# Kernel tuning notes

Measured on AMD Instinct MI355X. Metric: run time of the kernel, lower is better.

Reference implementation:

```python
import jax, jax.numpy as jnp
import numpy as np

DIM = 3
N_GRID = 128
DX = 1.0 / N_GRID
INV_DX = float(N_GRID)
DT = 1e-4
P_VOL = (DX * 0.5) ** 2
P_RHO = 1.0
P_MASS = P_VOL * P_RHO
E_MOD = 5000.0
NU = 0.2
MU0 = E_MOD / (2.0 * (1.0 + NU))
LAM0 = E_MOD * NU / ((1.0 + NU) * (1.0 - 2.0 * NU))
N_PARTICLES = 400_000

# 27 stencil offsets of the quadratic B-spline kernel
_OFF = jnp.array([[i, j, k] for i in range(3) for j in range(3) for k in range(3)],
                 dtype=jnp.int32)  # [27,3]


def _substep(x, v, C, F, Jp, gravity, attractor_strength, attractor_pos, material):
    N = x.shape[0]
    dtype = x.dtype
    I3 = jnp.eye(3, dtype=dtype)

    # ---- particle -> grid (P2G) ----
    base = jnp.floor(x * INV_DX - 0.5).astype(jnp.int32)          # [N,3]
    fx = x * INV_DX - base.astype(dtype)                          # [N,3]
    # quadratic kernel weights, w[a, n, d], a in {0,1,2}
    w = jnp.stack([0.5 * (1.5 - fx) ** 2,
                   0.75 - (fx - 1.0) ** 2,
                   0.5 * (fx - 0.5) ** 2], axis=0)                # [3,N,3]

    Fn = jnp.einsum('nij,njk->nik', I3 + DT * C, F)               # deformation update

    h = jnp.clip(jnp.exp(10.0 * (1.0 - Jp)), 0.1, 5.0)
    h = jnp.where(material == 1, 0.3, h)
    mu = jnp.where(material == 0, 0.0, MU0 * h)                   # [N]
    la = LAM0 * h                                                 # [N]

    U, s, Vh = jnp.linalg.svd(Fn, full_matrices=False)            # [N,3,3],[N,3],[N,3,3]

    # faithful to source: plasticity loop only touches first TWO singular values
    J = jnp.ones_like(Jp)
    sig = s
    for d in range(2):
        new_sig = jnp.where(material == 2,
                            jnp.clip(s[:, d], 1.0 - 0.025, 1.0 + 0.0045),
                            s[:, d])
        Jp = Jp * s[:, d] / new_sig
        sig = sig.at[:, d].set(new_sig)
        J = J * new_sig

    F_fluid = jnp.sqrt(J)[:, None, None] * I3                     # material 0
    F_snow = jnpum = None
    F_snow = jnp.einsum('nij,nj,njk->nik', U, sig, Vh)            # material 2: U diag(sig) V^T
    m3 = material[:, None, None]
    Fn = jnp.where(m3 == 0, F_fluid, jnp.where(m3 == 2, F_snow, Fn))

    R = jnp.einsum('nij,njk->nik', U, Vh)                         # U V^T (rotation)
    stress = (2.0 * mu[:, None, None] * jnp.einsum('nij,nkj->nik', Fn - R, Fn)
              + I3 * (la * J * (J - 1.0))[:, None, None])
    stress = (-DT * P_VOL * 4.0 * INV_DX * INV_DX) * stress
    affine = stress + P_MASS * C                                  # [N,3,3]

    # NOTE faithful quirk of the source: weight = w[i][0] * w[j][1] (k-component unused)
    weight = w[_OFF[:, 0], :, 0] * w[_OFF[:, 1], :, 1]            # [27,N]
    dpos = (_OFF[:, None, :].astype(dtype) - fx[None]) * DX       # [27,N,3]
    mom = weight[..., None] * (P_MASS * v[None]
                               + jnp.einsum('nij,onj->oni', affine, dpos))  # [27,N,3]

    idx = base[None] + _OFF[:, None, :]                           # [27,N,3]
    flat = (idx[..., 0] * N_GRID + idx[..., 1]) * N_GRID + idx[..., 2]      # [27,N]
    G3 = N_GRID ** 3
    grid_mom = jnp.zeros((G3, 3), dtype).at[flat.reshape(-1)].add(mom.reshape(-1, 3))
    grid_m = jnp.zeros((G3,), dtype).at[flat.reshape(-1)].add((weight * P_MASS).reshape(-1))

    # ---- grid update ----
    a = jnp.arange(N_GRID, dtype=jnp.int32)
    coords = jnp.stack(jnp.meshgrid(a, a, a, indexing='ij'), axis=-1).reshape(G3, 3)
    mask = grid_m > 0
    m_safe = jnp.where(mask, grid_m, 1.0)
    gv = grid_mom / m_safe[:, None]
    gv = gv + DT * gravity * 30.0
    dist = attractor_pos[None, :] - DX * coords.astype(dtype)
    gv = gv + dist / (0.01 + jnp.linalg.norm(dist, axis=-1, keepdims=True)) \
              * attractor_strength * DT * 100.0
    ic, jc = coords[:, 0], coords[:, 1]
    vx, vy, vz = gv[:, 0], gv[:, 1], gv[:, 2]
    vx = jnp.where((ic < 3) & (vx < 0), 0.0, vx)
    vx = jnp.where((ic > N_GRID - 3) & (vx > 0), 0.0, vx)
    vy = jnp.where((jc < 3) & (vy < 0), 0.0, vy)
    vy = jnp.where((jc > N_GRID - 3) & (vy > 0), 0.0, vy)
    gv = jnp.stack([vx, vy, vz], axis=-1)
    gv = jnp.where(mask[:, None], gv, 0.0)                        # untouched cells stay zero

    # ---- grid -> particle (G2P) ----
    g_v = gv[flat]                                                # [27,N,3]
    dpos2 = _OFF[:, None, :].astype(dtype) - fx[None]             # [27,N,3] (no dx scale)
    new_v = jnp.einsum('on,onc->nc', weight, g_v)                 # [N,3]
    new_C = 4.0 * INV_DX * jnp.einsum('on,onc,ond->ncd', weight, g_v, dpos2)  # [N,3,3]
    x_new = x + DT * new_v

    # pack state: [x(3) | v(3) | Jp(1) | F(9) | C(9)] -> [N,25]
    return jnp.concatenate([x_new, new_v, Jp[:, None],
                            Fn.reshape(N, 9), new_C.reshape(N, 9)], axis=1)


def setup_inputs() -> dict:
    key = jax.random.key(0)
    ks = jax.random.split(key, 9)
    N = N_PARTICLES
    x = 0.1 + 0.8 * jax.random.uniform(ks[0], (N, 3), dtype=jnp.float32)
    v = 0.1 * jax.random.normal(ks[1], (N, 3), dtype=jnp.float32)
    C = 0.01 * jax.random.normal(ks[2], (N, 3, 3), dtype=jnp.float32)
    F = jnp.eye(3, dtype=jnp.float32) + 0.01 * jax.random.normal(ks[3], (N, 3, 3), dtype=jnp.float32)
    Jp = 1.0 + 0.1 * jax.random.uniform(ks[4], (N,), dtype=jnp.float32)
    material = jax.random.randint(ks[5], (N,), 0, 3, dtype=jnp.int32)
    gravity = jnp.array([0.0, -1.0, 0.0], dtype=jnp.float32)
    attractor_strength = jax.random.uniform(ks[6], (), dtype=jnp.float32)
    attractor_pos = jax.random.uniform(ks[7], (3,), dtype=jnp.float32)
    return {"x": x, "v": v, "C": C, "F": F, "Jp": Jp,
            "gravity": gravity, "attractor_strength": attractor_strength,
            "attractor_pos": attractor_pos, "material": material}


def reference(x, v, C, F, Jp, gravity, attractor_strength, attractor_pos, material):
    return _substep(x, v, C, F, Jp, gravity, attractor_strength, attractor_pos, material)
```

## Files before the change

kernel.cpp:

```cpp
#include <hip/hip_runtime.h>

#define NG 128
#define G3 (NG*NG*NG)
#define NSCAN_BLOCKS (G3/256)

__device__ __constant__ const float c_DX      = 1.0f/128.0f;
__device__ __constant__ const float c_INV_DX  = 128.0f;

#define DT      1e-4f
#define P_VOL   ((1.0f/256.0f)*(1.0f/256.0f))
#define P_MASS  P_VOL
#define MU0     (5000.0f/(2.0f*1.2f))
#define LAM0    (5000.0f*0.2f/(1.2f*0.6f))

struct __align__(16) PRec {
    float4 r0, r1, r2, r3;
};

template<int P, int Q>
__device__ inline void jacobi_rot(float S[3][3], float V[3][3]) {
    float apq = S[P][Q];
    if (fabsf(apq) < 1e-24f) return;
    float tau = (S[Q][Q] - S[P][P]) / (2.0f * apq);
    float t = copysignf(1.0f, tau) / (fabsf(tau) + sqrtf(1.0f + tau*tau));
    float c = rsqrtf(1.0f + t*t);
    float sn = t * c;
    #pragma unroll
    for (int k = 0; k < 3; ++k) {
        float Spk = S[P][k], Sqk = S[Q][k];
        S[P][k] = c*Spk - sn*Sqk;
        S[Q][k] = sn*Spk + c*Sqk;
    }
    #pragma unroll
    for (int k = 0; k < 3; ++k) {
        float Skp = S[k][P], Skq = S[k][Q];
        S[k][P] = c*Skp - sn*Skq;
        S[k][Q] = sn*Skp + c*Skq;
    }
    #pragma unroll
    for (int k = 0; k < 3; ++k) {
        float Vkp = V[k][P], Vkq = V[k][Q];
        V[k][P] = c*Vkp - sn*Vkq;
        V[k][Q] = sn*Vkp + c*Vkq;
    }
}

#define CSWAPF(cond, x, y) { float _t = (x); (x) = (cond) ? (y) : (x); (y) = (cond) ? _t : (y); }

__device__ inline void svd3(const float A[9], float U[9], float sv[3], float V[9]) {
    float S[3][3];
    #pragma unroll
    for (int i = 0; i < 3; ++i)
        #pragma unroll
        for (int j = 0; j < 3; ++j) {
            float acc = 0.f;
            #pragma unroll
            for (int k = 0; k < 3; ++k) acc += A[k*3+i]*A[k*3+j];
            S[i][j] = acc;
        }
    float Vm[3][3] = {{1.f,0.f,0.f},{0.f,1.f,0.f},{0.f,0.f,1.f}};
    #pragma unroll
    for (int sweep = 0; sweep < 4; ++sweep) {
        jacobi_rot<0,1>(S, Vm);
        jacobi_rot<0,2>(S, Vm);
        jacobi_rot<1,2>(S, Vm);
    }
    float l0 = S[0][0], l1 = S[1][1], l2 = S[2][2];
    float a0 = Vm[0][0], b0 = Vm[1][0], c0 = Vm[2][0];
    float a1 = Vm[0][1], b1 = Vm[1][1], c1 = Vm[2][1];
    float a2 = Vm[0][2], b2 = Vm[1][2], c2 = Vm[2][2];
    bool s01 = l0 < l1;
    CSWAPF(s01, l0, l1) CSWAPF(s01, a0, a1) CSWAPF(s01, b0, b1) CSWAPF(s01, c0, c1)
    bool s02 = l0 < l2;
    CSWAPF(s02, l0, l2) CSWAPF(s02, a0, a2) CSWAPF(s02, b0, b2) CSWAPF(s02, c0, c2)
    bool s12 = l1 < l2;
    CSWAPF(s12, l1, l2) CSWAPF(s12, a1, a2) CSWAPF(s12, b1, b2) CSWAPF(s12, c1, c2)

    {
        float l = fmaxf(l0, 0.f); float sval = sqrtf(l); sv[0] = sval;
        V[0] = a0; V[3] = b0; V[6] = c0;
        float inv = (sval > 1e-12f) ? 1.0f/sval : 0.f;
        U[0] = (A[0]*a0 + A[1]*b0 + A[2]*c0)*inv;
        U[3] = (A[3]*a0 + A[4]*b0 + A[5]*c0)*inv;
        U[6] = (A[6]*a0 + A[7]*b0 + A[8]*c0)*inv;
    }
    {
        float l = fmaxf(l1, 0.f); float sval = sqrtf(l); sv[1] = sval;
        V[1] = a1; V[4] = b1; V[7] = c1;
        float inv = (sval > 1e-12f) ? 1.0f/sval : 0.f;
        U[1] = (A[0]*a1 + A[1]*b1 + A[2]*c1)*inv;
        U[4] = (A[3]*a1 + A[4]*b1 + A[5]*c1)*inv;
        U[7] = (A[6]*a1 + A[7]*b1 + A[8]*c1)*inv;
    }
    {
        float l = fmaxf(l2, 0.f); float sval = sqrtf(l); sv[2] = sval;
        V[2] = a2; V[5] = b2; V[8] = c2;
        float inv = (sval > 1e-12f) ? 1.0f/sval : 0.f;
        U[2] = (A[0]*a2 + A[1]*b2 + A[2]*c2)*inv;
        U[5] = (A[3]*a2 + A[4]*b2 + A[5]*c2)*inv;
        U[8] = (A[6]*a2 + A[7]*b2 + A[8]*c2)*inv;
    }
}

__device__ inline void base_from_A(float A0, float A1, float A2,
                                   int& bi, int& bj, int& bk,
                                   float& fx0, float& fx1, float& fx2) {
    float bxf = floorf(A0 - 0.5f);
    float byf = floorf(A1 - 0.5f);
    float bzf = floorf(A2 - 0.5f);
    bi = (int)bxf; bj = (int)byf; bk = (int)bzf;
    bi = min(max(bi, 0), NG-3); bj = min(max(bj, 0), NG-3); bk = min(max(bk, 0), NG-3);
    fx0 = A0 - bxf;
    fx1 = A1 - byf;
    fx2 = A2 - bzf;
}

__global__ void __launch_bounds__(256)
count_kernel(const float* __restrict__ x, int* __restrict__ cell_count,
             int* __restrict__ rank, int N) {
    int n = blockIdx.x*256 + threadIdx.x;
    if (n >= N) return;
    int bi, bj, bk; float f0, f1, f2;
    base_from_A(x[3*n+0]*c_INV_DX, x[3*n+1]*c_INV_DX, x[3*n+2]*c_INV_DX,
                bi, bj, bk, f0, f1, f2);
    rank[n] = atomicAdd(&cell_count[(bi*NG + bj)*NG + bk], 1);
}

__global__ void __launch_bounds__(256)
scan_partial_kernel(const int* __restrict__ count, int* __restrict__ partial) {
    __shared__ int red[256];
    int t = threadIdx.x;
    red[t] = count[blockIdx.x*256 + t];
    __syncthreads();
    for (int off = 128; off > 0; off >>= 1) {
        if (t < off) red[t] += red[t+off];
        __syncthreads();
    }
    if (t == 0) partial[blockIdx.x] = red[0];
}

__global__ void __launch_bounds__(256)
scan_partials_kernel(int* __restrict__ partial) {
    __shared__ int part[256];
    int t = threadIdx.x;
    int base = t*32;
    int local[32];
    int s = 0;
    #pragma unroll
    for (int i = 0; i < 32; ++i) { local[i] = s; s += partial[base+i]; }
    part[t] = s;
    __syncthreads();
    for (int off = 1; off < 256; off <<= 1) {
        int v = (t >= off) ? part[t-off] : 0;
        __syncthreads();
        part[t] += v;
        __syncthreads();
    }
    int prev = (t == 0) ? 0 : part[t-1];
    #pragma unroll
    for (int i = 0; i < 32; ++i) partial[base+i] = prev + local[i];
}

__global__ void __launch_bounds__(256)
scan_final_kernel(const int* __restrict__ count, const int* __restrict__ partial,
                  int* __restrict__ offset) {
    __shared__ int part[256];
    int t = threadIdx.x;
    int i = blockIdx.x*256 + t;
    int c = count[i];
    part[t] = c;
    __syncthreads();
    for (int off = 1; off < 256; off <<= 1) {
        int v = (t >= off) ? part[t-off] : 0;
        __syncthreads();
        part[t] += v;
        __syncthreads();
    }
    int base = partial[blockIdx.x];
    offset[i] = base + part[t] - c;
    if (i == G3-1) offset[G3] = base + part[t];
}

__global__ void __launch_bounds__(256)
pre_kernel(const float* __restrict__ x, const float* __restrict__ v,
           const float* __restrict__ Cin, const float* __restrict__ Fin,
           const float* __restrict__ Jp_in, const int* __restrict__ material,
           const int* __restrict__ offset, const int* __restrict__ rank,
           PRec* __restrict__ rec, float* __restrict__ out, int N) {
    int n = blockIdx.x*256 + threadIdx.x;
    if (n >= N) return;

    float A0 = x[3*n+0]*c_INV_DX, A1 = x[3*n+1]*c_INV_DX, A2 = x[3*n+2]*c_INV_DX;
    int bi, bj, bk; float f0, f1, f2;
    base_from_A(A0, A1, A2, bi, bj, bk, f0, f1, f2);

    float Cm[9], Fm[9];
    #pragma unroll
    for (int i = 0; i < 9; ++i) { Cm[i] = Cin[9*n+i]; Fm[i] = Fin[9*n+i]; }

    float Fn[9];
    #pragma unroll
    for (int i = 0; i < 3; ++i)
        #pragma unroll
        for (int k = 0; k < 3; ++k) {
            float acc = Fm[i*3+k];
            #pragma unroll
            for (int j = 0; j < 3; ++j) acc += DT * Cm[i*3+j] * Fm[j*3+k];
            Fn[i*3+k] = acc;
        }

    float Jp = Jp_in[n];
    int mat = material[n];
    float h = expf(10.0f*(1.0f - Jp));
    h = fminf(fmaxf(h, 0.1f), 5.0f);
    if (mat == 1) h = 0.3f;
    float mu = (mat == 0) ? 0.0f : MU0*h;
    float la = LAM0*h;

    float U[9], V[9], sv[3];
    svd3(Fn, U, sv, V);

    float J = 1.0f;
    float sig[3];
    #pragma unroll
    for (int d = 0; d < 2; ++d) {
        float s = sv[d];
        float ns = (mat == 2) ? fminf(fmaxf(s, 1.0f-0.025f), 1.0f+0.0045f) : s;
        Jp = Jp * s / ns;
        sig[d] = ns;
        J *= ns;
    }
    sig[2] = sv[2];

    if (mat == 0) {
        float sj = sqrtf(J);
        Fn[0]=sj; Fn[1]=0; Fn[2]=0; Fn[3]=0; Fn[4]=sj; Fn[5]=0; Fn[6]=0; Fn[7]=0; Fn[8]=sj;
    } else if (mat == 2) {
        #pragma unroll
        for (int i = 0; i < 3; ++i)
            #pragma unroll
            for (int k = 0; k < 3; ++k) {
                float acc = 0.f;
                #pragma unroll
                for (int j = 0; j < 3; ++j) acc += U[i*3+j]*sig[j]*V[k*3+j];
                Fn[i*3+k] = acc;
            }
    }

    float R[9];
    #pragma unroll
    for (int i = 0; i < 3; ++i)
        #pragma unroll
        for (int k = 0; k < 3; ++k) {
            float acc = 0.f;
            #pragma unroll
            for (int j = 0; j < 3; ++j) acc += U[i*3+j]*V[k*3+j];
            R[i*3+k] = acc;
        }

    float press = la * J * (J - 1.0f);
    float scale = -DT * P_VOL * 4.0f * c_INV_DX * c_INV_DX;
    float aff[9];
    #pragma unroll
    for (int i = 0; i < 3; ++i)
        #pragma unroll
        for (int k = 0; k < 3; ++k) {
            float acc = 0.f;
            #pragma unroll
            for (int j = 0; j < 3; ++j) acc += (Fn[i*3+j]-R[i*3+j])*Fn[k*3+j];
            acc = 2.0f*mu*acc;
            if (i == k) acc += press;
            aff[i*3+k] = scale*acc + P_MASS*Cm[i*3+k];
        }

    float* po = out + (size_t)n*25;
    po[6] = Jp;
    #pragma unroll
    for (int i = 0; i < 9; ++i) po[7+i] = Fn[i];

    int cell = (bi*NG + bj)*NG + bk;
    int pos = offset[cell] + rank[n];

    float4* rp = (float4*)&rec[pos];
    rp[0] = make_float4(A0, A1, A2, __int_as_float(n));
    rp[1] = make_float4(aff[0], aff[1], aff[2], aff[3]);
    rp[2] = make_float4(aff[4], aff[5], aff[6], aff[7]);
    rp[3] = make_float4(aff[8], P_MASS*v[3*n+0], P_MASS*v[3*n+1], P_MASS*v[3*n+2]);
}

__global__ void __launch_bounds__(128)
grid_gather_kernel(const PRec* __restrict__ rec, const int* __restrict__ offset,
                   float4* __restrict__ grid, const float* __restrict__ gravity,
                   const float* __restrict__ attr_s, const float* __restrict__ attr_p) {
    __shared__ int rS[9*128];
    __shared__ int rE[9*128];
    int tid = threadIdx.x;
    int g4 = blockIdx.x*128 + tid;
    int zq = g4 & 31;
    int gj = (g4 >> 5) & (NG-1);
    int gi = g4 >> 12;
    int zlo = zq*4;

    int bk0 = max(zlo-2, 0), bk1 = min(zlo+3, NG-3);

    bool any = false;
    #pragma unroll
    for (int di = 0; di < 3; ++di) {
        int bi = gi - 2 + di;
        bool vi = (bi >= 0) && (bi <= NG-3);
        #pragma unroll
        for (int dj = 0; dj < 3; ++dj) {
            int bj = gj - 2 + dj;
            bool vj = vi && (bj >= 0) && (bj <= NG-3);
            int col = ((vj ? bi : 0)*NG + (vj ? bj : 0))*NG;
            int s = vj ? offset[col + bk0]     : 0;
            int e = vj ? offset[col + bk1 + 1] : 0;
            rS[(di*3+dj)*128 + tid] = s;
            rE[(di*3+dj)*128 + tid] = e;
            if (s < e) any = true;
        }
    }

    if (!any) return;

    float ax[4], ay[4], az[4], mm[4];
    #pragma unroll
    for (int h = 0; h < 4; ++h) { ax[h]=0.f; ay[h]=0.f; az[h]=0.f; mm[h]=0.f; }

    float gif = (float)gi, gjf = (float)gj, z0f = (float)zlo;

    int ridx = 0;
    int p = rS[tid], e = rE[tid];
    while (p >= e) {
        if (++ridx >= 9) break;
        p = rS[ridx*128 + tid]; e = rE[ridx*128 + tid];
    }
    while (ridx < 9) {
        const float4* rp = (const float4*)&rec[p];
        float4 r0 = rp[0];
        float4 r1 = rp[1];
        float4 r2 = rp[2];
        float4 r3 = rp[3];

        float ux = gif - r0.x;
        float aux = fabsf(ux);
        float tx = 1.5f - aux;
        float nx = (aux < 0.5f) ? (0.75f - ux*ux) : (0.5f*tx*tx);
        float uy = gjf - r0.y;
        float auy = fabsf(uy);
        float ty = 1.5f - auy;
        float ny = (auy < 0.5f) ? (0.75f - uy*uy) : (0.5f*ty*ty);
        float wgt = nx*ny;

        float uz0 = z0f - r0.z;
        float dpx = ux*c_DX, dpy = uy*c_DX, dpz0 = uz0*c_DX;
        float cx = r3.y + r1.x*dpx + r1.y*dpy + r1.z*dpz0;
        float cy = r3.z + r1.w*dpx + r2.x*dpy + r2.y*dpz0;
        float cz = r3.w + r2.z*dpx + r2.w*dpy + r3.x*dpz0;
        float ix = r1.z*c_DX, iy = r2.y*c_DX, iz = r3.x*c_DX;

        #pragma unroll
        for (int h = 0; h < 4; ++h) {
            float uz = uz0 + (float)h;
            float w = (uz > -1.5f && uz <= 1.5f) ? wgt : 0.f;
            ax[h] += w*cx; ay[h] += w*cy; az[h] += w*cz; mm[h] += w*P_MASS;
            cx += ix; cy += iy; cz += iz;
        }

        ++p;
        while (p >= e) {
            if (++ridx >= 9) break;
            p = rS[ridx*128 + tid]; e = rE[ridx*128 + tid];
        }
    }

    float gx = DT*gravity[0]*30.0f, gy = DT*gravity[1]*30.0f, gz = DT*gravity[2]*30.0f;
    float apx = attr_p[0], apy = attr_p[1], apz = attr_p[2];
    float as  = attr_s[0] * DT * 100.0f;

    int gidx = (gi*NG + gj)*NG + zlo;
    #pragma unroll
    for (int h = 0; h < 4; ++h) {
        float m = mm[h];
        int gk = zlo + h;
        float gvx = 0.f, gvy = 0.f, gvz = 0.f;
        if (m > 0.f) {
            float inv = 1.0f/m;
            gvx = ax[h]*inv + gx; gvy = ay[h]*inv + gy; gvz = az[h]*inv + gz;
            float dx_ = apx - c_DX*(float)gi;
            float dy_ = apy - c_DX*(float)gj;
            float dz_ = apz - c_DX*(float)gk;
            float nrm = sqrtf(dx_*dx_ + dy_*dy_ + dz_*dz_);
            float sc = as / (0.01f + nrm);
            gvx += dx_*sc; gvy += dy_*sc; gvz += dz_*sc;
            if (gi < 3      && gvx < 0.f) gvx = 0.f;
            if (gi > NG-3   && gvx > 0.f) gvx = 0.f;
            if (gj < 3      && gvy < 0.f) gvy = 0.f;
            if (gj > NG-3   && gvy > 0.f) gvy = 0.f;
        }
        grid[gidx + h] = make_float4(gvx, gvy, gvz, m);
    }
}

__global__ void __launch_bounds__(256)
g2p_kernel(const PRec* __restrict__ rec, const float4* __restrict__ grid,
           float* __restrict__ out, int N) {
    int gid = blockIdx.x * 256 + threadIdx.x;
    if (gid >= N) return;

    float4 r0 = rec[gid].r0;
    float A0 = r0.x, A1 = r0.y, A2 = r0.z;
    int n = __float_as_int(r0.w);

    int bi, bj, bk; float fx0, fx1, fx2;
    base_from_A(A0, A1, A2, bi, bj, bk, fx0, fx1, fx2);

    float wx[3], wy[3];
    wx[0] = 0.5f*(1.5f-fx0)*(1.5f-fx0); wx[1] = 0.75f-(fx0-1.f)*(fx0-1.f); wx[2] = 0.5f*(fx0-0.5f)*(fx0-0.5f);
    wy[0] = 0.5f*(1.5f-fx1)*(1.5f-fx1); wy[1] = 0.75f-(fx1-1.f)*(fx1-1.f); wy[2] = 0.5f*(fx1-0.5f)*(fx1-0.5f);

    float nvx = 0.f, nvy = 0.f, nvz = 0.f;
    float nC[9];
    #pragma unroll
    for (int i = 0; i < 9; ++i) nC[i] = 0.f;

    #pragma unroll
    for (int i = 0; i < 3; ++i) {
        float dpx = (float)i - fx0;
        #pragma unroll
        for (int j = 0; j < 3; ++j) {
            float wgt = wx[i]*wy[j];
            float dpy = (float)j - fx1;
            int cell0 = ((bi+i)*NG + (bj+j))*NG + bk;
            #pragma unroll
            for (int k = 0; k < 3; ++k) {
                float dpz = (float)k - fx2;
                float4 gv = grid[cell0 + k];
                float wgx = wgt*gv.x, wgy = wgt*gv.y, wgz = wgt*gv.z;
                nvx += wgx; nvy += wgy; nvz += wgz;
                nC[0] += wgx*dpx; nC[1] += wgx*dpy; nC[2] += wgx*dpz;
                nC[3] += wgy*dpx; nC[4] += wgy*dpy; nC[5] += wgy*dpz;
                nC[6] += wgz*dpx; nC[7] += wgz*dpy; nC[8] += wgz*dpz;
            }
        }
    }

    float* po = out + (size_t)n*25;
    float px = A0*c_DX, py = A1*c_DX, pz = A2*c_DX;
    po[0] = px + DT*nvx;
    po[1] = py + DT*nvy;
    po[2] = pz + DT*nvz;
    po[3] = nvx; po[4] = nvy; po[5] = nvz;
    float s4 = 4.0f*c_INV_DX;
    #pragma unroll
    for (int i = 0; i < 9; ++i) po[16+i] = s4*nC[i];
}

extern "C" void kernel_launch(void* const* d_in, const int* in_sizes, int n_in,
                              void* d_out, int out_size, void* d_ws, size_t ws_size,
                              hipStream_t stream) {
    const float* x        = (const float*)d_in[0];
    const float* v        = (const float*)d_in[1];
    const float* C        = (const float*)d_in[2];
    const float* F        = (const float*)d_in[3];
    const float* Jp       = (const float*)d_in[4];
    const float* gravity  = (const float*)d_in[5];
    const float* attr_s   = (const float*)d_in[6];
    const float* attr_p   = (const float*)d_in[7];
    const int*   material = (const int*)d_in[8];
    float* out = (float*)d_out;
    int N = in_sizes[0] / 3;

    char* ws = (char*)d_ws;
    size_t o = 0;
    int* cell_count = (int*)(ws + o);      o += (size_t)G3*sizeof(int);
    size_t zero_bytes = o;
    int* offset     = (int*)(ws + o);      o += ((size_t)G3+1)*sizeof(int);
    int* partial    = (int*)(ws + o);      o += (size_t)NSCAN_BLOCKS*sizeof(int);
    int* rank       = (int*)(ws + o);      o += (size_t)N*sizeof(int);
    o = (o + 127) & ~(size_t)127;
    float4* grid    = (float4*)(ws + o);   o += (size_t)G3*sizeof(float4);
    PRec* rec       = (PRec*)(ws + o);     o += (size_t)N*sizeof(PRec);

    hipMemsetAsync(d_ws, 0, zero_bytes, stream);

    int pblocks = (N + 255) / 256;
    count_kernel<<<pblocks, 256, 0, stream>>>(x, cell_count, rank, N);
    scan_partial_kernel<<<NSCAN_BLOCKS, 256, 0, stream>>>(cell_count, partial);
    scan_partials_kernel<<<1, 256, 0, stream>>>(partial);
    scan_final_kernel<<<NSCAN_BLOCKS, 256, 0, stream>>>(cell_count, partial, offset);
    pre_kernel<<<pblocks, 256, 0, stream>>>(x, v, C, F, Jp, material,
                                            offset, rank, rec, out, N);
    grid_gather_kernel<<<G3/512, 128, 0, stream>>>(rec, offset, grid,
                                                   gravity, attr_s, attr_p);
    g2p_kernel<<<pblocks, 256, 0, stream>>>(rec, grid, out, N);
}
```

Measured before the change: 261.8 us.

## Replace three-kernel prefix scan with single-pass decoupled lookback scan

Merges the partial-reduce, partials-scan and final-scan kernels into one kernel that uses dynamic block tickets and decoupled lookback. Each block publishes its aggregate, then its inclusive prefix, in a per-block state word. This removes two kernel launches and one extra read pass over the 2M-cell count array. It adds serial lookback spinning by one thread per block and needs 8192 state words zeroed by the memset.

```diff
diff --git a/kernel.cpp b/kernel.cpp
--- a/kernel.cpp
+++ b/kernel.cpp
@@ -127,47 +127,19 @@
 }
 
 __global__ void __launch_bounds__(256)
-scan_partial_kernel(const int* __restrict__ count, int* __restrict__ partial) {
-    __shared__ int red[256];
+scan_lookback_kernel(const int* __restrict__ count, int* __restrict__ offset,
+                     unsigned long long* __restrict__ state,
+                     int* __restrict__ ticket) {
+    __shared__ int part[256];
+    __shared__ int sh_bid;
+    __shared__ int sh_prefix;
     int t = threadIdx.x;
-    red[t] = count[blockIdx.x*256 + t];
+    if (t == 0) sh_bid = atomicAdd(ticket, 1);
     __syncthreads();
-    for (int off = 128; off > 0; off >>= 1) {
-        if (t < off) red[t] += red[t+off];
-        __syncthreads();
-    }
-    if (t == 0) partial[blockIdx.x] = red[0];
-}
-
-__global__ void __launch_bounds__(256)
-scan_partials_kernel(int* __restrict__ partial) {
-    __shared__ int part[256];
-    int t = threadIdx.x;
-    int base = t*32;
-    int local[32];
-    int s = 0;
-    #pragma unroll
-    for (int i = 0; i < 32; ++i) { local[i] = s; s += partial[base+i]; }
-    part[t] = s;
-    __syncthreads();
-    for (int off = 1; off < 256; off <<= 1) {
-        int v = (t >= off) ? part[t-off] : 0;
-        __syncthreads();
-        part[t] += v;
-        __syncthreads();
-    }
-    int prev = (t == 0) ? 0 : part[t-1];
-    #pragma unroll
-    for (int i = 0; i < 32; ++i) partial[base+i] = prev + local[i];
-}
-
-__global__ void __launch_bounds__(256)
-scan_final_kernel(const int* __restrict__ count, const int* __restrict__ partial,
-                  int* __restrict__ offset) {
-    __shared__ int part[256];
-    int t = threadIdx.x;
-    int i = blockIdx.x*256 + t;
+    int bid = sh_bid;
+    int i = bid*256 + t;
     int c = count[i];
+
     part[t] = c;
     __syncthreads();
     for (int off = 1; off < 256; off <<= 1) {
@@ -176,9 +148,30 @@
         part[t] += v;
         __syncthreads();
     }
-    int base = partial[blockIdx.x];
-    offset[i] = base + part[t] - c;
-    if (i == G3-1) offset[G3] = base + part[t];
+    int incl = part[t];
+    int aggregate = part[255];
+
+    if (t == 0) {
+        atomicExch(&state[bid], (1ULL << 32) | (unsigned int)aggregate);
+        int prefix = 0;
+        int prev = bid - 1;
+        while (prev >= 0) {
+            unsigned long long st;
+            do {
+                st = atomicAdd(&state[prev], 0ULL);
+            } while ((st >> 32) == 0ULL);
+            int val = (int)(st & 0xffffffffULL);
+            if ((st >> 32) == 2ULL) { prefix += val; break; }
+            prefix += val;
+            --prev;
+        }
+        atomicExch(&state[bid], (2ULL << 32) | (unsigned int)(prefix + aggregate));
+        sh_prefix = prefix;
+    }
+    __syncthreads();
+    int base = sh_prefix;
+    offset[i] = base + incl - c;
+    if (i == G3-1) offset[G3] = base + incl;
 }
 
 __global__ void __launch_bounds__(256)
@@ -473,22 +466,23 @@
 
     char* ws = (char*)d_ws;
     size_t o = 0;
-    int* cell_count = (int*)(ws + o);      o += (size_t)G3*sizeof(int);
+    int* cell_count = (int*)(ws + o);              o += (size_t)G3*sizeof(int);
+    unsigned long long* state = (unsigned long long*)(ws + o);
+                                                   o += (size_t)NSCAN_BLOCKS*sizeof(unsigned long long);
+    int* ticket     = (int*)(ws + o);              o += 128;
     size_t zero_bytes = o;
-    int* offset     = (int*)(ws + o);      o += ((size_t)G3+1)*sizeof(int);
-    int* partial    = (int*)(ws + o);      o += (size_t)NSCAN_BLOCKS*sizeof(int);
-    int* rank       = (int*)(ws + o);      o += (size_t)N*sizeof(int);
+    int* offset     = (int*)(ws + o);              o += ((size_t)G3+1)*sizeof(int);
+    int* rank       = (int*)(ws + o);              o += (size_t)N*sizeof(int);
     o = (o + 127) & ~(size_t)127;
-    float4* grid    = (float4*)(ws + o);   o += (size_t)G3*sizeof(float4);
-    PRec* rec       = (PRec*)(ws + o);     o += (size_t)N*sizeof(PRec);
+    float4* grid    = (float4*)(ws + o);           o += (size_t)G3*sizeof(float4);
+    PRec* rec       = (PRec*)(ws + o);             o += (size_t)N*sizeof(PRec);
 
     hipMemsetAsync(d_ws, 0, zero_bytes, stream);
 
     int pblocks = (N + 255) / 256;
     count_kernel<<<pblocks, 256, 0, stream>>>(x, cell_count, rank, N);
-    scan_partial_kernel<<<NSCAN_BLOCKS, 256, 0, stream>>>(cell_count, partial);
-    scan_partials_kernel<<<1, 256, 0, stream>>>(partial);
-    scan_final_kernel<<<NSCAN_BLOCKS, 256, 0, stream>>>(cell_count, partial, offset);
+    scan_lookback_kernel<<<NSCAN_BLOCKS, 256, 0, stream>>>(cell_count, offset,
+                                                           state, ticket);
     pre_kernel<<<pblocks, 256, 0, stream>>>(x, v, C, F, Jp, material,
                                             offset, rank, rec, out, N);
     grid_gather_kernel<<<G3/512, 128, 0, stream>>>(rec, offset, grid,
```

Measured after the change: 367.8 us. 1.4x slower.
